# Kernel tuning notes

Hardware: AMD Instinct MI355X
Metric: run time of the kernel (lower is better)

Reference implementation:

```python
import jax, jax.numpy as jnp
import numpy as np

D_MODEL = 2048
NUM_HEADS = 32
NUM_KV_HEADS = 8
HEAD_DIM = D_MODEL // NUM_HEADS  # 64
B, S = 2, 2048


def rotary_cos_sin(seq_len, head_dim, dtype=jnp.float32):
    inv_freq = 1.0 / (10000.0 ** (jnp.arange(0, head_dim, 2, dtype=jnp.float32) / head_dim))
    t = jnp.arange(seq_len, dtype=jnp.float32)
    freqs = t[:, None] * inv_freq[None, :]          # [S, hd/2]
    emb = jnp.concatenate([freqs, freqs], axis=-1)  # [S, hd]
    return emb.astype(dtype).reshape(1, seq_len, 1, head_dim), None  # placeholder


def apply_rotary_emb(x, cos, sin):
    # faithful to source: interleaved rotate-half, concatenated cos/sin
    x1 = x[..., ::2]
    x2 = x[..., 1::2]
    rotated = jnp.stack([-x2, x1], axis=-1).reshape(x.shape)
    return x * cos + rotated * sin


def setup_inputs() -> dict:
    key = jax.random.key(0)
    ks = jax.random.split(key, 5)
    sc = 0.02
    x = jax.random.normal(ks[0], (B, S, D_MODEL), dtype=jnp.float32)
    Wq = jax.random.normal(ks[1], (D_MODEL, D_MODEL), dtype=jnp.float32) * sc
    Wk = jax.random.normal(ks[2], (D_MODEL, NUM_KV_HEADS * HEAD_DIM), dtype=jnp.float32) * sc
    Wv = jax.random.normal(ks[3], (D_MODEL, NUM_KV_HEADS * HEAD_DIM), dtype=jnp.float32) * sc
    Wo = jax.random.normal(ks[4], (D_MODEL, D_MODEL), dtype=jnp.float32) * sc
    mask = jnp.tril(jnp.ones((S, S), dtype=jnp.int32))[None, None]  # [1,1,S,S] causal
    return {"x": x, "mask": mask, "Wq": Wq, "Wk": Wk, "Wv": Wv, "Wo": Wo}


def reference(x, mask, Wq, Wk, Wv, Wo):
    b, s, _ = x.shape
    q = (x @ Wq).reshape(b, s, NUM_HEADS, HEAD_DIM)
    k = (x @ Wk).reshape(b, s, NUM_KV_HEADS, HEAD_DIM)
    v = (x @ Wv).reshape(b, s, NUM_KV_HEADS, HEAD_DIM)

    inv_freq = 1.0 / (10000.0 ** (jnp.arange(0, HEAD_DIM, 2, dtype=jnp.float32) / HEAD_DIM))
    t = jnp.arange(s, dtype=jnp.float32)
    freqs = t[:, None] * inv_freq[None, :]
    emb = jnp.concatenate([freqs, freqs], axis=-1)         # [S, hd]
    cos = jnp.cos(emb)[None, :, None, :].astype(x.dtype)   # [1,S,1,hd]
    sin = jnp.sin(emb)[None, :, None, :].astype(x.dtype)

    q = apply_rotary_emb(q, cos, sin)
    k = apply_rotary_emb(k, cos, sin)

    rep = NUM_HEADS // NUM_KV_HEADS
    k = jnp.repeat(k, rep, axis=2)  # [B,S,H,hd]
    v = jnp.repeat(v, rep, axis=2)

    q = q.transpose(0, 2, 1, 3)  # [B,H,S,hd]
    k = k.transpose(0, 2, 1, 3)
    v = v.transpose(0, 2, 1, 3)

    scale = 1.0 / jnp.sqrt(jnp.asarray(HEAD_DIM, dtype=x.dtype))
    scores = jnp.einsum('bhqd,bhkd->bhqk', q, k) * scale
    scores = jnp.where(mask == 0, jnp.asarray(-jnp.inf, scores.dtype), scores)
    attn = jax.nn.softmax(scores, axis=-1)
    out = jnp.einsum('bhqk,bhkd->bhqd', attn, v)
    out = out.transpose(0, 2, 1, 3).reshape(b, s, D_MODEL)
    return out @ Wo
```

## Files before the change

### kernel.cpp

```cpp
#include <hip/hip_runtime.h>
#include <hip/hip_bf16.h>

typedef __bf16 bf16;
typedef __bf16 bf16x8 __attribute__((ext_vector_type(8)));
typedef float  f32x4  __attribute__((ext_vector_type(4)));

#define B_  2
#define S_  2048
#define H_  32
#define HK_ 8
#define D_  64
#define DM_ 2048
#define LDQ 3072

__device__ __forceinline__ void async_copy16(const bf16* g, bf16* l) {
    __builtin_amdgcn_global_load_lds((const __attribute__((address_space(1))) void*)g,
                                     (__attribute__((address_space(3))) void*)l,
                                     16, 0, 0);
}

__global__ __launch_bounds__(256) void convert_x(const float* __restrict__ in,
                                                 bf16* __restrict__ out) {
    const long i = (long)blockIdx.x * 256 + threadIdx.x;
    const float4 v = ((const float4*)in)[i];
    bf16* o = out + i * 4;
    o[0] = (bf16)v.x; o[1] = (bf16)v.y; o[2] = (bf16)v.z; o[3] = (bf16)v.w;
}

__global__ __launch_bounds__(256) void transpose2d(const float* __restrict__ in,
                                                   bf16* __restrict__ out,
                                                   int R, int C) {
    __shared__ bf16 tile[32][33];
    const int tx = threadIdx.x & 31;
    const int ty = threadIdx.x >> 5;
    const long r0 = (long)blockIdx.y * 32;
    const long c0 = (long)blockIdx.x * 32;
#pragma unroll
    for (int k = 0; k < 4; ++k)
        tile[ty + 8 * k][tx] = (bf16)in[(r0 + ty + 8 * k) * C + c0 + tx];
    __syncthreads();
#pragma unroll
    for (int k = 0; k < 4; ++k)
        out[(c0 + ty + 8 * k) * R + r0 + tx] = tile[tx][ty + 8 * k];
}

__global__ __launch_bounds__(256) void v_transpose(const bf16* __restrict__ qkv,
                                                   bf16* __restrict__ out) {
    __shared__ bf16 tile[32][33];
    const int p = blockIdx.z;
    const int b = p >> 3, h = p & 7;
    const int s0 = blockIdx.x * 32;
    const int d0 = blockIdx.y * 32;
    const int tx = threadIdx.x & 31;
    const int ty = threadIdx.x >> 5;
    const bf16* ip = qkv + (long)(b * S_) * LDQ + 2560 + h * 64;
#pragma unroll
    for (int k = 0; k < 4; ++k)
        tile[ty + 8 * k][tx] = ip[(long)(s0 + ty + 8 * k) * LDQ + d0 + tx];
    __syncthreads();
    bf16* op = out + ((long)(b * HK_ + h) * D_) * S_;
#pragma unroll
    for (int k = 0; k < 4; ++k)
        op[(long)(d0 + ty + 8 * k) * S_ + s0 + tx] = tile[tx][ty + 8 * k];
}

__global__ __launch_bounds__(256) void rope_all(bf16* qkv) {
    const int idx = blockIdx.x * 256 + threadIdx.x;
    const int i  = idx & 31;
    const int s  = (idx >> 5) & (S_ - 1);
    const int ord = idx >> 16;
    const int b  = (ord >= 40) ? 1 : 0;
    const int hh = ord - 40 * b;
    const int colOff = (hh < 32) ? hh * 64 : 2048 + (hh - 32) * 64;
    const long base = (long)(b * S_ + s) * LDQ + colOff;
    const float x0 = (float)qkv[base + 2 * i];
    const float x1 = (float)qkv[base + 2 * i + 1];
    const float t = (float)s;
    const float c10k = 9.210340371976184f;
    const int i0 = (2 * i) & 31;
    const int i1 = (2 * i + 1) & 31;
    const float f0 = t * expf(-(float)i0 * (c10k / 32.f));
    const float f1 = t * expf(-(float)i1 * (c10k / 32.f));
    const float o0 = x0 * cosf(f0) - x1 * sinf(f0);
    const float o1 = x1 * cosf(f1) + x0 * sinf(f1);
    qkv[base + 2 * i]     = (bf16)o0;
    qkv[base + 2 * i + 1] = (bf16)o1;
}

template <typename OutT>
__global__ __launch_bounds__(512) void gemm_bt8(const bf16* __restrict__ A, int lda,
                                                const bf16* __restrict__ Bt, int ldb,
                                                OutT* __restrict__ C, int ldc, int K) {
    constexpr int ABUF = 128 * 64;
    constexpr int BBUF = 256 * 64;
    constexpr int BUF  = ABUF + BBUF;
    __shared__ __align__(16) bf16 lds[3 * BUF];

    const int tid  = threadIdx.x;
    const int w    = tid >> 6;
    const int lane = tid & 63;
    const int quad = lane >> 4;
    const int l16  = lane & 15;
    const int x7   = l16 & 7;
    const int r8   = lane >> 3;
    const int sw8  = ((lane & 7) ^ r8) * 8;

    const int nwg  = gridDim.x * gridDim.y;
    const int bid  = blockIdx.y * gridDim.x + blockIdx.x;
    const int work = (bid & 7) * (nwg >> 3) + (bid >> 3);
    const long m0  = (long)(work / gridDim.x) * 128;
    const long n0  = (long)(work % gridDim.x) * 256;

    const int wr = w >> 2, wc = w & 3;

    bf16* p0 = lds;
    bf16* p1 = lds + BUF;
    bf16* p2 = lds + 2 * BUF;

    const bf16* Ag = A  + (m0 + w * 16 + r8) * lda + sw8;
    const bf16* Bg = Bt + (n0 + w * 32 + r8) * ldb + sw8;

#define SA(dst, ko, t) async_copy16(Ag + (long)(t) * 8 * lda + (ko), (dst) + (w * 16 + (t) * 8) * 64)
#define SB(dst, ko, t) async_copy16(Bg + (long)(t) * 8 * ldb + (ko), (dst) + ABUF + (w * 32 + (t) * 8) * 64)
#define LA(buf, m, ks) (*(const bf16x8*)((buf) + (wr * 64 + (m) * 16 + l16) * 64 + ((((ks) * 4 + quad) ^ x7) * 8)))
#define LB(buf, n, ks) (*(const bf16x8*)((buf) + ABUF + (wc * 64 + (n) * 16 + l16) * 64 + ((((ks) * 4 + quad) ^ x7) * 8)))

    SA(p0, 0, 0); SB(p0, 0, 0); SA(p0, 0, 1); SB(p0, 0, 1); SB(p0, 0, 2); SB(p0, 0, 3);
    SA(p1, 64, 0); SB(p1, 64, 0); SA(p1, 64, 1); SB(p1, 64, 1); SB(p1, 64, 2); SB(p1, 64, 3);

    f32x4 acc[4][4] = {};
    const int nt = K / 64;

    for (int t = 0; t < nt; ++t) {
        if (t < nt - 1) { asm volatile("s_waitcnt vmcnt(6)" ::: "memory"); }
        else            { asm volatile("s_waitcnt vmcnt(0)" ::: "memory"); }
        __builtin_amdgcn_s_barrier();
        __builtin_amdgcn_sched_barrier(0);
        const bool doStage = (t + 2 < nt);
        const int ko = (t + 2) * 64;
        bf16x8 af[4][2];
#pragma unroll
        for (int p = 0; p < 4; ++p) {
            if (p == 0) {
#pragma unroll
                for (int m = 0; m < 4; ++m) { af[m][0] = LA(p0, m, 0); af[m][1] = LA(p0, m, 1); }
            }
            const bf16x8 bb0 = LB(p0, p, 0);
            const bf16x8 bb1 = LB(p0, p, 1);
            if (doStage) {
                if (p == 1) { SA(p2, ko, 0); SB(p2, ko, 0); }
                if (p == 2) { SA(p2, ko, 1); SB(p2, ko, 1); }
                if (p == 3) { SB(p2, ko, 2); SB(p2, ko, 3); }
            }
            __builtin_amdgcn_s_barrier();
            __builtin_amdgcn_sched_barrier(0);
            __builtin_amdgcn_s_setprio(1);
#pragma unroll
            for (int m = 0; m < 4; ++m)
                acc[m][p] = __builtin_amdgcn_mfma_f32_16x16x32_bf16(af[m][0], bb0, acc[m][p], 0, 0, 0);
#pragma unroll
            for (int m = 0; m < 4; ++m)
                acc[m][p] = __builtin_amdgcn_mfma_f32_16x16x32_bf16(af[m][1], bb1, acc[m][p], 0, 0, 0);
            __builtin_amdgcn_s_setprio(0);
            __builtin_amdgcn_s_barrier();
            __builtin_amdgcn_sched_barrier(0);
        }
        bf16* tp = p0; p0 = p1; p1 = p2; p2 = tp;
    }
#undef SA
#undef SB
#undef LA
#undef LB

#pragma unroll
    for (int m = 0; m < 4; ++m) {
        const long r = m0 + wr * 64 + m * 16 + quad * 4;
#pragma unroll
        for (int n = 0; n < 4; ++n) {
            const long c = n0 + wc * 64 + n * 16 + l16;
#pragma unroll
            for (int reg = 0; reg < 4; ++reg)
                C[(r + reg) * ldc + c] = (OutT)acc[m][n][reg];
        }
    }
}

__global__ __launch_bounds__(256, 4) void attn_fused(bf16* qkv,
                                                     const bf16* __restrict__ Vt) {
    __shared__ __align__(16) bf16 Ks[64 * 64];
    __shared__ __align__(16) bf16 Vs[64 * 64];
    __shared__ __align__(16) bf16 Pbuf[4][32 * 72];
    const int tid  = threadIdx.x;
    const int w    = tid >> 6;
    const int lane = tid & 63;
    const int quad = lane >> 4;
    const int l16  = lane & 15;
    const int r8   = lane >> 3;
    const int sw   = (lane & 7) ^ r8;
    const int x7   = l16 & 7;

    const int bid = blockIdx.x;
    const int grp = bid & 15;
    const int qi  = 63 - (bid >> 4);
    const int hk  = grp & 7;
    const int b   = grp >> 3;
    const int h   = hk * 4 + w;

    const bf16* kp = qkv + (long)(b * S_) * LDQ + 2048 + hk * 64;
    const bf16* vp = Vt + (long)(b * HK_ + hk) * D_ * S_;
    bf16* P = &Pbuf[w][0];

    const float C1 = 0.18033688011112043f;
    const float C2 = 23.083120654223415f;
    const f32x4 zero = {0.f, 0.f, 0.f, 0.f};

    const int q0 = qi * 32;
    bf16* qp = qkv + (long)(b * S_ + q0) * LDQ + h * 64;

    bf16x8 aq[2][2];
#pragma unroll
    for (int i = 0; i < 2; ++i)
#pragma unroll
        for (int half = 0; half < 2; ++half)
            aq[i][half] = *(const bf16x8*)(qp + (long)(i * 16 + l16) * LDQ + half * 32 + quad * 8);

    f32x4 accO[2][4] = {};
    float ps[2][4] = {};

    const int nkt = q0 / 64 + 1;
    for (int kt = 0; kt < nkt; ++kt) {
        const int kb = kt * 64;
        __syncthreads();
#pragma unroll
        for (int t = 0; t < 2; ++t) {
            const int rloc = w * 16 + t * 8;
            async_copy16(kp + (long)(kb + rloc + r8) * LDQ + sw * 8, Ks + rloc * 64);
            async_copy16(vp + (long)(rloc + r8) * S_ + kb + sw * 8,  Vs + rloc * 64);
        }
        __syncthreads();

        const bool lastTile = (kt == nkt - 1);
#pragma unroll
        for (int g = 0; g < 4; ++g) {
            const int krow = g * 16 + l16;
            const bf16x8 bk0 = *(const bf16x8*)(Ks + krow * 64 + ((quad ^ x7) * 8));
            const bf16x8 bk1 = *(const bf16x8*)(Ks + krow * 64 + (((quad + 4) ^ x7) * 8));
#pragma unroll
            for (int i = 0; i < 2; ++i) {
                __builtin_amdgcn_s_setprio(1);
                f32x4 t = __builtin_amdgcn_mfma_f32_16x16x32_bf16(aq[i][0], bk0, zero, 0, 0, 0);
                f32x4 s = __builtin_amdgcn_mfma_f32_16x16x32_bf16(aq[i][1], bk1, t, 0, 0, 0);
                __builtin_amdgcn_s_setprio(0);
#pragma unroll
                for (int rg = 0; rg < 4; ++rg) {
                    float e;
                    if (lastTile) {
                        const int key  = kb + g * 16 + l16;
                        const int qrow = q0 + i * 16 + quad * 4 + rg;
                        e = (key <= qrow)
                          ? __builtin_amdgcn_exp2f(fminf(s[rg] * C1 - C2, 10.f)) : 0.f;
                    } else {
                        e = __builtin_amdgcn_exp2f(fminf(s[rg] * C1 - C2, 10.f));
                    }
                    ps[i][rg] += e;
                    P[(i * 16 + quad * 4 + rg) * 72 + g * 16 + l16] = (bf16)e;
                }
            }
        }
        __asm__ volatile("s_waitcnt lgkmcnt(0)" ::: "memory");
#pragma unroll
        for (int i = 0; i < 2; ++i) {
            const bf16x8 aP0 = *(const bf16x8*)(P + (i * 16 + l16) * 72 + quad * 8);
            const bf16x8 aP1 = *(const bf16x8*)(P + (i * 16 + l16) * 72 + 32 + quad * 8);
#pragma unroll
            for (int c = 0; c < 4; ++c) {
                const int vrow = c * 16 + l16;
                const bf16x8 bv0 = *(const bf16x8*)(Vs + vrow * 64 + ((quad ^ x7) * 8));
                const bf16x8 bv1 = *(const bf16x8*)(Vs + vrow * 64 + (((quad + 4) ^ x7) * 8));
                __builtin_amdgcn_s_setprio(1);
                accO[i][c] = __builtin_amdgcn_mfma_f32_16x16x32_bf16(aP0, bv0, accO[i][c], 0, 0, 0);
                accO[i][c] = __builtin_amdgcn_mfma_f32_16x16x32_bf16(aP1, bv1, accO[i][c], 0, 0, 0);
                __builtin_amdgcn_s_setprio(0);
            }
        }
        __asm__ volatile("s_waitcnt lgkmcnt(0)" ::: "memory");
    }

#pragma unroll
    for (int off = 1; off < 16; off <<= 1)
#pragma unroll
        for (int i = 0; i < 2; ++i)
#pragma unroll
            for (int rg = 0; rg < 4; ++rg)
                ps[i][rg] += __shfl_xor(ps[i][rg], off, 64);
    float invl[2][4];
#pragma unroll
    for (int i = 0; i < 2; ++i)
#pragma unroll
        for (int rg = 0; rg < 4; ++rg) invl[i][rg] = 1.f / ps[i][rg];

#pragma unroll
    for (int i = 0; i < 2; ++i)
#pragma unroll
        for (int c = 0; c < 4; ++c)
#pragma unroll
            for (int rg = 0; rg < 4; ++rg) {
                const long row = (long)(b * S_ + q0 + i * 16 + quad * 4 + rg);
                qkv[row * LDQ + h * 64 + c * 16 + l16] = (bf16)(accO[i][c][rg] * invl[i][rg]);
            }
}

extern "C" void kernel_launch(void* const* d_in, const int* in_sizes, int n_in,
                              void* d_out, int out_size, void* d_ws, size_t ws_size,
                              hipStream_t stream) {
    (void)in_sizes; (void)n_in; (void)out_size; (void)ws_size;
    const float* x  = (const float*)d_in[0];
    const float* Wq = (const float*)d_in[2];
    const float* Wk = (const float*)d_in[3];
    const float* Wv = (const float*)d_in[4];
    const float* Wo = (const float*)d_in[5];
    float* out = (float*)d_out;

    bf16* qkv = (bf16*)d_ws;
    bf16* wT3 = qkv + 4096L * 3072;
    bf16* xb  = (bf16*)d_out;
    bf16* vT  = xb + 4096L * 2048;

    const dim3 blk(256);

    convert_x<<<dim3(8388608 / (256 * 4)), blk, 0, stream>>>(x, xb);

    transpose2d<<<dim3(64, 64), blk, 0, stream>>>(Wq, wT3, 2048, 2048);
    transpose2d<<<dim3(16, 64), blk, 0, stream>>>(Wk, wT3 + 2048L * 2048, 2048, 512);
    transpose2d<<<dim3(16, 64), blk, 0, stream>>>(Wv, wT3 + 2560L * 2048, 2048, 512);

    gemm_bt8<bf16><<<dim3(12, 32), dim3(512), 0, stream>>>(
        xb, 2048, wT3, 2048, qkv, LDQ, 2048);

    rope_all<<<dim3((B_ * (H_ + HK_) * S_ * 32) / 256), blk, 0, stream>>>(qkv);
    v_transpose<<<dim3(S_ / 32, D_ / 32, B_ * HK_), blk, 0, stream>>>(qkv, vT);

    attn_fused<<<dim3(B_ * HK_ * 64), blk, 0, stream>>>(qkv, vT);

    transpose2d<<<dim3(64, 64), blk, 0, stream>>>(Wo, wT3, 2048, 2048);
    gemm_bt8<float><<<dim3(8, 32), dim3(512), 0, stream>>>(
        qkv, LDQ, wT3, 2048, out, 2048, 2048);
}
```

Measured before the change: 327.8 us.

## Replace 128x256 8-wave GEMM with 128x128 4-wave tile and K=32 stages

The projection GEMMs move from a 512-thread kernel with 128x256 tiles and K=64 stages to a 256-thread kernel with 128x128 tiles, K=32 stages, a new LDS swizzle and a simpler per-iteration schedule with an occupancy hint of 3 blocks. The grouped block-index remapping for L2 locality is dropped in favour of plain blockIdx ordering. The aim is more blocks in flight and less barrier overhead per K step. The cost is lower data reuse per tile, more global traffic and more loop iterations.

```diff
diff --git a/kernel.cpp b/kernel.cpp
--- a/kernel.cpp
+++ b/kernel.cpp
@@ -88,12 +88,11 @@
 }
 
 template <typename OutT>
-__global__ __launch_bounds__(512) void gemm_bt8(const bf16* __restrict__ A, int lda,
-                                                const bf16* __restrict__ Bt, int ldb,
-                                                OutT* __restrict__ C, int ldc, int K) {
-    constexpr int ABUF = 128 * 64;
-    constexpr int BBUF = 256 * 64;
-    constexpr int BUF  = ABUF + BBUF;
+__global__ __launch_bounds__(256, 3) void gemm_tb(const bf16* __restrict__ A, int lda,
+                                                  const bf16* __restrict__ Bt, int ldb,
+                                                  OutT* __restrict__ C, int ldc, int K) {
+    constexpr int ABUF = 128 * 32;
+    constexpr int BUF  = 2 * ABUF;
     __shared__ __align__(16) bf16 lds[3 * BUF];
 
     const int tid  = threadIdx.x;
@@ -101,76 +100,61 @@
     const int lane = tid & 63;
     const int quad = lane >> 4;
     const int l16  = lane & 15;
-    const int x7   = l16 & 7;
-    const int r8   = lane >> 3;
-    const int sw8  = ((lane & 7) ^ r8) * 8;
-
-    const int nwg  = gridDim.x * gridDim.y;
-    const int bid  = blockIdx.y * gridDim.x + blockIdx.x;
-    const int work = (bid & 7) * (nwg >> 3) + (bid >> 3);
-    const long m0  = (long)(work / gridDim.x) * 128;
-    const long n0  = (long)(work % gridDim.x) * 256;
-
-    const int wr = w >> 2, wc = w & 3;
+    const int wr   = w >> 1;
+    const int wc   = w & 1;
+    const long m0  = (long)blockIdx.y * 128;
+    const long n0  = (long)blockIdx.x * 128;
+
+    const int srow = lane >> 2;
+    const int schk = ((lane & 3) ^ ((lane >> 3) & 3)) * 8;
+    const bf16* Ag = A  + (m0 + w * 32 + srow) * lda + schk;
+    const bf16* Bg = Bt + (n0 + w * 32 + srow) * ldb + schk;
+
+    const int rchk = (quad ^ ((l16 >> 1) & 3)) * 8;
+    const int aoff = (wr * 64 + l16) * 32 + rchk;
+    const int boff = (wc * 64 + l16) * 32 + rchk;
+
+#define STAGE(buf, k0)                                                          \
+    do {                                                                        \
+        async_copy16(Ag + (k0),            (buf) + (w * 32) * 32);              \
+        async_copy16(Ag + 16 * lda + (k0), (buf) + (w * 32 + 16) * 32);         \
+        async_copy16(Bg + (k0),            (buf) + ABUF + (w * 32) * 32);       \
+        async_copy16(Bg + 16 * ldb + (k0), (buf) + ABUF + (w * 32 + 16) * 32);  \
+    } while (0)
 
     bf16* p0 = lds;
     bf16* p1 = lds + BUF;
     bf16* p2 = lds + 2 * BUF;
 
-    const bf16* Ag = A  + (m0 + w * 16 + r8) * lda + sw8;
-    const bf16* Bg = Bt + (n0 + w * 32 + r8) * ldb + sw8;
-
-#define SA(dst, ko, t) async_copy16(Ag + (long)(t) * 8 * lda + (ko), (dst) + (w * 16 + (t) * 8) * 64)
-#define SB(dst, ko, t) async_copy16(Bg + (long)(t) * 8 * ldb + (ko), (dst) + ABUF + (w * 32 + (t) * 8) * 64)
-#define LA(buf, m, ks) (*(const bf16x8*)((buf) + (wr * 64 + (m) * 16 + l16) * 64 + ((((ks) * 4 + quad) ^ x7) * 8)))
-#define LB(buf, n, ks) (*(const bf16x8*)((buf) + ABUF + (wc * 64 + (n) * 16 + l16) * 64 + ((((ks) * 4 + quad) ^ x7) * 8)))
-
-    SA(p0, 0, 0); SB(p0, 0, 0); SA(p0, 0, 1); SB(p0, 0, 1); SB(p0, 0, 2); SB(p0, 0, 3);
-    SA(p1, 64, 0); SB(p1, 64, 0); SA(p1, 64, 1); SB(p1, 64, 1); SB(p1, 64, 2); SB(p1, 64, 3);
+    STAGE(p0, 0);
+    STAGE(p1, 32);
 
     f32x4 acc[4][4] = {};
-    const int nt = K / 64;
+    const int nt = K / 32;
 
     for (int t = 0; t < nt; ++t) {
-        if (t < nt - 1) { asm volatile("s_waitcnt vmcnt(6)" ::: "memory"); }
+        if (t < nt - 1) { asm volatile("s_waitcnt vmcnt(4)" ::: "memory"); }
         else            { asm volatile("s_waitcnt vmcnt(0)" ::: "memory"); }
         __builtin_amdgcn_s_barrier();
         __builtin_amdgcn_sched_barrier(0);
-        const bool doStage = (t + 2 < nt);
-        const int ko = (t + 2) * 64;
-        bf16x8 af[4][2];
-#pragma unroll
-        for (int p = 0; p < 4; ++p) {
-            if (p == 0) {
-#pragma unroll
-                for (int m = 0; m < 4; ++m) { af[m][0] = LA(p0, m, 0); af[m][1] = LA(p0, m, 1); }
-            }
-            const bf16x8 bb0 = LB(p0, p, 0);
-            const bf16x8 bb1 = LB(p0, p, 1);
-            if (doStage) {
-                if (p == 1) { SA(p2, ko, 0); SB(p2, ko, 0); }
-                if (p == 2) { SA(p2, ko, 1); SB(p2, ko, 1); }
-                if (p == 3) { SB(p2, ko, 2); SB(p2, ko, 3); }
-            }
-            __builtin_amdgcn_s_barrier();
-            __builtin_amdgcn_sched_barrier(0);
-            __builtin_amdgcn_s_setprio(1);
-#pragma unroll
-            for (int m = 0; m < 4; ++m)
-                acc[m][p] = __builtin_amdgcn_mfma_f32_16x16x32_bf16(af[m][0], bb0, acc[m][p], 0, 0, 0);
-#pragma unroll
-            for (int m = 0; m < 4; ++m)
-                acc[m][p] = __builtin_amdgcn_mfma_f32_16x16x32_bf16(af[m][1], bb1, acc[m][p], 0, 0, 0);
-            __builtin_amdgcn_s_setprio(0);
-            __builtin_amdgcn_s_barrier();
-            __builtin_amdgcn_sched_barrier(0);
-        }
+        if (t + 2 < nt) STAGE(p2, (t + 2) * 32);
+        bf16x8 a[4], b[4];
+#pragma unroll
+        for (int m = 0; m < 4; ++m) a[m] = *(const bf16x8*)(p0 + aoff + m * 16 * 32);
+#pragma unroll
+        for (int n = 0; n < 4; ++n) b[n] = *(const bf16x8*)(p0 + ABUF + boff + n * 16 * 32);
+        asm volatile("s_waitcnt lgkmcnt(0)" ::: "memory");
+        __builtin_amdgcn_sched_barrier(0);
+        __builtin_amdgcn_s_setprio(1);
+#pragma unroll
+        for (int m = 0; m < 4; ++m)
+#pragma unroll
+            for (int n = 0; n < 4; ++n)
+                acc[m][n] = __builtin_amdgcn_mfma_f32_16x16x32_bf16(a[m], b[n], acc[m][n], 0, 0, 0);
+        __builtin_amdgcn_s_setprio(0);
         bf16* tp = p0; p0 = p1; p1 = p2; p2 = tp;
     }
-#undef SA
-#undef SB
-#undef LA
-#undef LB
+#undef STAGE
 
 #pragma unroll
     for (int m = 0; m < 4; ++m) {
@@ -334,7 +318,7 @@
     transpose2d<<<dim3(16, 64), blk, 0, stream>>>(Wk, wT3 + 2048L * 2048, 2048, 512);
     transpose2d<<<dim3(16, 64), blk, 0, stream>>>(Wv, wT3 + 2560L * 2048, 2048, 512);
 
-    gemm_bt8<bf16><<<dim3(12, 32), dim3(512), 0, stream>>>(
+    gemm_tb<bf16><<<dim3(24, 32), blk, 0, stream>>>(
         xb, 2048, wT3, 2048, qkv, LDQ, 2048);
 
     rope_all<<<dim3((B_ * (H_ + HK_) * S_ * 32) / 256), blk, 0, stream>>>(qkv);
@@ -343,6 +327,6 @@
     attn_fused<<<dim3(B_ * HK_ * 64), blk, 0, stream>>>(qkv, vT);
 
     transpose2d<<<dim3(64, 64), blk, 0, stream>>>(Wo, wT3, 2048, 2048);
-    gemm_bt8<float><<<dim3(8, 32), dim3(512), 0, stream>>>(
+    gemm_tb<float><<<dim3(16, 32), blk, 0, stream>>>(
         qkv, LDQ, wT3, 2048, out, 2048, 2048);
 }
```

After: 318.5 us. -2.8%, faster.
